# Optimization experiments

Measured on AMD Instinct MI355X. Metric: run time of the kernel, lower is better.

The kernel has to match this reference:

```python
import jax, jax.numpy as jnp
import numpy as np

N_NODES = 50000
N_EDGES = 800000
DIMS = [128, 512, 256, 128]
EPS = 1e-5


def setup_inputs() -> dict:
    key = jax.random.key(0)
    ks = jax.random.split(key, 2 + 5 * 3)
    inp = {
        "x": jax.random.normal(ks[0], (N_NODES, DIMS[0]), dtype=jnp.float32),
        "edge_index": jax.random.randint(ks[1], (2, N_EDGES), 0, N_NODES, dtype=jnp.int64),
    }
    ki = 2
    for i in range(3):
        din, dout = DIMS[i], DIMS[i + 1]
        s = 1.0 / np.sqrt(din)
        inp[f"Wl{i}"] = jax.random.uniform(ks[ki + 0], (din, dout), jnp.float32, -s, s)
        inp[f"bl{i}"] = jax.random.uniform(ks[ki + 1], (dout,), jnp.float32, -s, s)
        inp[f"Wr{i}"] = jax.random.uniform(ks[ki + 2], (din, dout), jnp.float32, -s, s)
        inp[f"g{i}"] = jnp.ones((dout,), jnp.float32)
        inp[f"b{i}"] = jnp.zeros((dout,), jnp.float32)
        ki += 5
    return inp


def _sage_mean(x, src, dst, Wl, bl, Wr):
    n = x.shape[0]
    agg = jax.ops.segment_sum(x[src], dst, num_segments=n)  # [N, din]
    deg = jax.ops.segment_sum(jnp.ones((src.shape[0],), x.dtype), dst, num_segments=n)
    mean = agg / jnp.maximum(deg, 1.0)[:, None]
    return mean @ Wl + bl + x @ Wr


def _bn(h, gamma, beta):
    m = h.mean(axis=0)
    v = h.var(axis=0)
    return gamma * (h - m) * jax.lax.rsqrt(v + EPS) + beta


def reference(x, edge_index, Wl0, bl0, Wr0, g0, b0, Wl1, bl1, Wr1, g1, b1, Wl2, bl2, Wr2, g2, b2):
    src, dst = edge_index[0], edge_index[1]
    params = [(Wl0, bl0, Wr0, g0, b0), (Wl1, bl1, Wr1, g1, b1), (Wl2, bl2, Wr2, g2, b2)]
    h = x
    for Wl, bl, Wr, g, b in params:
        h = _sage_mean(h, src, dst, Wl, bl, Wr)
        h = _bn(h, g, b)
        h = jax.nn.relu(h)
        # dropout: identity in eval mode
    return h
```

## Files before the change

kernel.cpp:

```cpp
#include <hip/hip_runtime.h>
#include <cstdint>
#include <cstddef>


#define EPS_BN 1e-5f

typedef unsigned short ushort_t;
typedef __attribute__((ext_vector_type(8))) short short8;
typedef __attribute__((ext_vector_type(4))) float float4v;
typedef __attribute__((ext_vector_type(2))) float float2v;
typedef __attribute__((ext_vector_type(2))) unsigned int uint2v;
typedef __attribute__((ext_vector_type(4))) unsigned int uint4v;

__device__ __forceinline__ float bflo(unsigned int w) {
    union { unsigned int i; float f; } v; v.i = w << 16; return v.f;
}
__device__ __forceinline__ float bfhi(unsigned int w) {
    union { unsigned int i; float f; } v; v.i = w & 0xffff0000u; return v.f;
}
__device__ __forceinline__ ushort_t f2bf(float f) {
    union { float f; unsigned int i; } v; v.f = f;
    unsigned int r = v.i + 0x7fffu + ((v.i >> 16) & 1u);
    return (ushort_t)(r >> 16);
}

__device__ __forceinline__ void async_copy16(void* lds, const void* g) {
    __builtin_amdgcn_global_load_lds(
        (const __attribute__((address_space(1))) unsigned int*)g,
        (__attribute__((address_space(3))) unsigned int*)lds, 16, 0, 0);
}

__device__ __forceinline__ void edge_sd(const int* __restrict__ p, int e, int ne,
                                        bool is64, int& s, int& d) {
    if (is64) { s = p[2 * e];  d = p[2 * ne + 2 * e]; }
    else      { s = p[e];      d = p[ne + e]; }
}
__device__ __forceinline__ int edge_d(const int* __restrict__ p, int e, int ne, bool is64) {
    return is64 ? p[2 * ne + 2 * e] : p[ne + e];
}

__device__ __forceinline__ bool detect_is64(const int* __restrict__ edges,
                                            int* sh_flag, int t) {
    if (t == 0) *sh_flag = 1;
    __syncthreads();
    if (t < 64 && edges[2 * t + 1] != 0) *sh_flag = 0;
    __syncthreads();
    return *sh_flag != 0;
}

#define EPB 2048

__global__ __launch_bounds__(256) void bhist_kernel(
    const int* __restrict__ edges, int ne, int* __restrict__ gcnt) {
    __shared__ int h[256];
    __shared__ int f64;
    int t = threadIdx.x;
    bool is64 = detect_is64(edges, &f64, t);
    h[t] = 0;
    __syncthreads();
    int base_e = blockIdx.x * EPB;
    #pragma unroll
    for (int u = 0; u < EPB / 256; ++u) {
        int i = base_e + u * 256 + t;
        if (i < ne) atomicAdd(&h[edge_d(edges, i, ne, is64) >> 8], 1);
    }
    __syncthreads();
    if (h[t]) atomicAdd(&gcnt[t], h[t]);
}

__global__ __launch_bounds__(256) void bscan_kernel(
    const int* __restrict__ gcnt, int nb, int ne,
    int* __restrict__ bbase, int* __restrict__ bcur) {
    __shared__ int sh[256];
    int t = threadIdx.x;
    int v = (t < nb) ? gcnt[t] : 0;
    sh[t] = v;
    __syncthreads();
    for (int o = 1; o < 256; o <<= 1) {
        int x = (t >= o) ? sh[t - o] : 0;
        __syncthreads();
        sh[t] += x;
        __syncthreads();
    }
    int excl = sh[t] - v;
    if (t < nb) { bbase[t] = excl; bcur[t] = excl; }
    if (t == nb) bbase[t] = ne;
    if (t == 0 && nb == 256) bbase[256] = ne;
}

__global__ __launch_bounds__(256) void bscatter_kernel(
    const int* __restrict__ edges, int ne,
    int* __restrict__ bcur, int* __restrict__ packed) {
    __shared__ int h[256];
    __shared__ int chunkb[256];
    __shared__ int lcur[256];
    __shared__ int f64;
    int t = threadIdx.x;
    bool is64 = detect_is64(edges, &f64, t);
    h[t] = 0;
    lcur[t] = 0;
    __syncthreads();
    int base_e = blockIdx.x * EPB;
    int ent[EPB / 256], eb[EPB / 256];
    #pragma unroll
    for (int u = 0; u < EPB / 256; ++u) {
        int i = base_e + u * 256 + t;
        if (i < ne) {
            int s, d;
            edge_sd(edges, i, ne, is64, s, d);
            ent[u] = s | ((d & 255) << 24);
            eb[u] = d >> 8;
            atomicAdd(&h[eb[u]], 1);
        } else eb[u] = -1;
    }
    __syncthreads();
    if (h[t]) chunkb[t] = atomicAdd(&bcur[t], h[t]);
    __syncthreads();
    #pragma unroll
    for (int u = 0; u < EPB / 256; ++u) {
        if (eb[u] >= 0) {
            int lp = atomicAdd(&lcur[eb[u]], 1);
            packed[chunkb[eb[u]] + lp] = ent[u];
        }
    }
}

__global__ __launch_bounds__(256) void bbuild_kernel(
    const int* __restrict__ packed, const int* __restrict__ bbase,
    int* __restrict__ rowptr, int* __restrict__ csr_src, int n) {
    __shared__ int h[256];
    __shared__ int cur[256];
    int t = threadIdx.x;
    int bb = blockIdx.x;
    int base = bbase[bb], cnt = bbase[bb + 1] - base;
    h[t] = 0;
    __syncthreads();
    for (int i = t; i < cnt; i += 256)
        atomicAdd(&h[(unsigned)packed[base + i] >> 24], 1);
    __syncthreads();
    int v = h[t];
    for (int o = 1; o < 256; o <<= 1) {
        int x = (t >= o) ? h[t - o] : 0;
        __syncthreads();
        h[t] += x;
        __syncthreads();
    }
    int excl = h[t] - v;
    int node = bb * 256 + t;
    if (node <= n) rowptr[node] = base + excl;
    cur[t] = excl;
    __syncthreads();
    for (int i = t; i < cnt; i += 256) {
        int e = packed[base + i];
        int lp = atomicAdd(&cur[(unsigned)e >> 24], 1);
        csr_src[base + lp] = e & 0xffffff;
    }
}

__global__ void prep_all_kernel(
    const float* __restrict__ x, ushort_t* __restrict__ xb, int nxb,
    const float* __restrict__ Wl0, const float* __restrict__ Wr0,
    ushort_t* __restrict__ WT0, int nb0,
    const float* __restrict__ Wl1, const float* __restrict__ Wr1,
    ushort_t* __restrict__ WT1c, int nb1,
    const float* __restrict__ Wl2, const float* __restrict__ Wr2,
    ushort_t* __restrict__ WT2c) {
    const int D0 = 128, D1 = 512, D2 = 256, D3 = 128;
    int b = blockIdx.x;
    if (b < nxb) {
        int i = b * 256 + threadIdx.x;
        xb[i] = f2bf(x[i]);
        return;
    }
    b -= nxb;
    if (b < nb0) {
        int idx = b * 256 + threadIdx.x;
        int K2 = 2 * D0;
        int nn = idx / K2, k = idx - nn * K2;
        float v = (k < D0) ? Wl0[(size_t)k * D1 + nn] : Wr0[(size_t)(k - D0) * D1 + nn];
        WT0[idx] = f2bf(v);
        return;
    }
    b -= nb0;
    if (b < nb1) {
        int idx = b * 256 + threadIdx.x;
        int nn = idx / D1, k = idx - nn * D1;
        float v = (nn < D2) ? Wl1[(size_t)k * D2 + nn] : Wr1[(size_t)k * D2 + (nn - D2)];
        WT1c[idx] = f2bf(v);
        return;
    }
    b -= nb1;
    {
        int idx = b * 256 + threadIdx.x;
        int nn = idx / D2, k = idx - nn * D2;
        float v = (nn < D3) ? Wl2[(size_t)k * D3 + nn] : Wr2[(size_t)k * D3 + (nn - D3)];
        WT2c[idx] = f2bf(v);
    }
}

template <int VEC> struct VecT;
template <> struct VecT<2> { using T = unsigned int; };
template <> struct VecT<4> { using T = uint2v; };
template <> struct VecT<8> { using T = uint4v; };

template <int VEC>
__device__ __forceinline__ void vunpack(typename VecT<VEC>::T v, unsigned int* w) {
    if constexpr (VEC == 2) { w[0] = v; }
    else if constexpr (VEC == 4) { w[0] = v.x; w[1] = v.y; }
    else { w[0] = v.x; w[1] = v.y; w[2] = v.z; w[3] = v.w; }
}

template <int VEC>
__device__ __forceinline__ void vaccum(typename VecT<VEC>::T v, float* acc) {
    unsigned int w[VEC / 2];
    vunpack<VEC>(v, w);
    #pragma unroll
    for (int i = 0; i < VEC / 2; ++i) {
        acc[2 * i + 0] += bflo(w[i]);
        acc[2 * i + 1] += bfhi(w[i]);
    }
}

template <int VEC>
__device__ __forceinline__ void gather_sum(
    const ushort_t* __restrict__ base, const int* __restrict__ csr_src,
    int e0, int e1, int rstride, float* acc) {
    using VT = typename VecT<VEC>::T;
    int e = e0;
    for (; e + 16 <= e1; e += 16) {
        VT v[16];
        #pragma unroll
        for (int u = 0; u < 16; ++u)
            v[u] = *(const VT*)(base + (size_t)csr_src[e + u] * rstride);
        #pragma unroll
        for (int u = 0; u < 16; ++u) vaccum<VEC>(v[u], acc);
    }
    if (e + 8 <= e1) {
        VT v[8];
        #pragma unroll
        for (int u = 0; u < 8; ++u)
            v[u] = *(const VT*)(base + (size_t)csr_src[e + u] * rstride);
        #pragma unroll
        for (int u = 0; u < 8; ++u) vaccum<VEC>(v[u], acc);
        e += 8;
    }
    if (e + 4 <= e1) {
        VT v[4];
        #pragma unroll
        for (int u = 0; u < 4; ++u)
            v[u] = *(const VT*)(base + (size_t)csr_src[e + u] * rstride);
        #pragma unroll
        for (int u = 0; u < 4; ++u) vaccum<VEC>(v[u], acc);
        e += 4;
    }
    if (e + 2 <= e1) {
        VT v0 = *(const VT*)(base + (size_t)csr_src[e] * rstride);
        VT v1 = *(const VT*)(base + (size_t)csr_src[e + 1] * rstride);
        vaccum<VEC>(v0, acc); vaccum<VEC>(v1, acc);
        e += 2;
    }
    if (e < e1)
        vaccum<VEC>(*(const VT*)(base + (size_t)csr_src[e] * rstride), acc);
}

template <int VEC>
__global__ __launch_bounds__(256) void aggregate_wave_kernel(
    const ushort_t* __restrict__ h, ushort_t* __restrict__ mean,
    const int* __restrict__ rowptr, const int* __restrict__ csr_src, int nnodes) {
    const int din = VEC * 64;
    const int wave = threadIdx.x >> 6;
    const int lane = threadIdx.x & 63;
    const int wstride = gridDim.x * 4;
    using VT = typename VecT<VEC>::T;
    for (int wid = blockIdx.x * 4 + wave; wid < nnodes; wid += wstride) {
        int e0 = rowptr[wid], e1 = rowptr[wid + 1];
        float acc[VEC];
        #pragma unroll
        for (int i = 0; i < VEC; ++i) acc[i] = 0.f;
        gather_sum<VEC>(h + (size_t)lane * VEC, csr_src, e0, e1, din, acc);

        int deg = e1 - e0;
        float scale = 1.0f / (float)(deg > 1 ? deg : 1);
        unsigned int o[VEC / 2];
        #pragma unroll
        for (int i = 0; i < VEC / 2; ++i)
            o[i] = (unsigned int)f2bf(acc[2 * i] * scale) |
                   ((unsigned int)f2bf(acc[2 * i + 1] * scale) << 16);
        VT ov;
        if constexpr (VEC == 2) { ov = o[0]; }
        else if constexpr (VEC == 4) { ov.x = o[0]; ov.y = o[1]; }
        else { ov.x = o[0]; ov.y = o[1]; ov.z = o[2]; ov.w = o[3]; }
        *(VT*)(mean + (size_t)wid * din + (size_t)lane * VEC) = ov;
    }
}

template <int VEC>
__global__ __launch_bounds__(256) void aggregate_add_kernel(
    const ushort_t* __restrict__ PR, const float* __restrict__ bias,
    ushort_t* __restrict__ pre,
    const int* __restrict__ rowptr, const int* __restrict__ csr_src, int nnodes,
    float* __restrict__ gsum, float* __restrict__ gsq) {
    const int D = VEC * 64;
    const int stride = 2 * D;
    __shared__ float s_red[2][4][VEC * 64];
    const int wave = threadIdx.x >> 6;
    const int lane = threadIdx.x & 63;
    const int wstride = gridDim.x * 4;
    using VT = typename VecT<VEC>::T;

    float ssum[VEC], ssq[VEC];
    #pragma unroll
    for (int i = 0; i < VEC; ++i) { ssum[i] = 0.f; ssq[i] = 0.f; }

    for (int wid = blockIdx.x * 4 + wave; wid < nnodes; wid += wstride) {
        int e0 = rowptr[wid], e1 = rowptr[wid + 1];
        float acc[VEC];
        #pragma unroll
        for (int i = 0; i < VEC; ++i) acc[i] = 0.f;
        gather_sum<VEC>(PR + (size_t)lane * VEC, csr_src, e0, e1, stride, acc);

        int deg = e1 - e0;
        float scale = 1.0f / (float)(deg > 1 ? deg : 1);

        VT rv = __builtin_nontemporal_load((const VT*)(PR + (size_t)wid * stride + D + (size_t)lane * VEC));
        unsigned int rw[VEC / 2];
        vunpack<VEC>(rv, rw);
        float o[VEC];
        #pragma unroll
        for (int i = 0; i < VEC / 2; ++i) {
            o[2 * i + 0] = bflo(rw[i]);
            o[2 * i + 1] = bfhi(rw[i]);
        }
        #pragma unroll
        for (int i = 0; i < VEC; ++i) {
            o[i] += acc[i] * scale + bias[lane * VEC + i];
            ssum[i] += o[i];
            ssq[i] += o[i] * o[i];
        }

        unsigned int ow[VEC / 2];
        #pragma unroll
        for (int i = 0; i < VEC / 2; ++i)
            ow[i] = (unsigned int)f2bf(o[2 * i]) | ((unsigned int)f2bf(o[2 * i + 1]) << 16);
        VT ov;
        if constexpr (VEC == 2) { ov = ow[0]; }
        else if constexpr (VEC == 4) { ov.x = ow[0]; ov.y = ow[1]; }
        else { ov.x = ow[0]; ov.y = ow[1]; ov.z = ow[2]; ov.w = ow[3]; }
        __builtin_nontemporal_store(ov, (VT*)(pre + (size_t)wid * D + (size_t)lane * VEC));
    }

    #pragma unroll
    for (int i = 0; i < VEC; ++i) {
        s_red[0][wave][lane * VEC + i] = ssum[i];
        s_red[1][wave][lane * VEC + i] = ssq[i];
    }
    __syncthreads();
    int t = threadIdx.x;
    if (t < D) {
        float a = s_red[0][0][t] + s_red[0][1][t] + s_red[0][2][t] + s_red[0][3][t];
        float q = s_red[1][0][t] + s_red[1][1][t] + s_red[1][2][t] + s_red[1][3][t];
        atomicAdd(&gsum[t], a);
        atomicAdd(&gsq[t], q);
    }
}

template <bool DUAL, bool BIAS, bool STATS>
__global__ __launch_bounds__(512) void gemm_glds_kernel(
    const ushort_t* __restrict__ A1, const ushort_t* __restrict__ A2,
    const ushort_t* __restrict__ BT, const float* __restrict__ bias,
    ushort_t* __restrict__ Cb, int N, int K1, int Ktot, int Wtot,
    float* __restrict__ gsum, float* __restrict__ gsq) {
    __shared__ ushort_t As[256 * 64];
    __shared__ ushort_t Bs[128 * 64];

    const int tid = threadIdx.x;
    const int wave = tid >> 6;
    const int lane = tid & 63;
    const int quad = lane >> 4;
    const int l15 = lane & 15;
    const int sw7 = l15 & 7;
    const int rowBase = blockIdx.y * 256;
    const int colBase = blockIdx.x * 128;
    const int wm = (wave >> 1) * 64;
    const int wn = (wave & 1) * 64;

    float4v acc[4][4];
    #pragma unroll
    for (int i = 0; i < 4; ++i)
        #pragma unroll
        for (int j = 0; j < 4; ++j)
            acc[i][j] = (float4v){0.f, 0.f, 0.f, 0.f};

    const int nkt = Ktot / 64;
    const int khalf = K1 / 64;

    for (int kt = 0; kt < nkt; ++kt) {
        const ushort_t* Asrc = A1;
        int kg = kt * 64;
        if (DUAL && kt >= khalf) { Asrc = A2; kg = (kt - khalf) * 64; }
        const int kb = kt * 64;

        #pragma unroll
        for (int u = 0; u < 4; ++u) {
            int c = u * 512 + tid;
            int r = c >> 3, cc = c & 7;
            int off = (cc ^ (r & 7)) * 8;
            int grow = rowBase + r;
            if (grow >= N) grow = N - 1;
            async_copy16(&As[c * 8], Asrc + (size_t)grow * K1 + kg + off);
        }
        #pragma unroll
        for (int u = 0; u < 2; ++u) {
            int c = u * 512 + tid;
            int r = c >> 3, cc = c & 7;
            int off = (cc ^ (r & 7)) * 8;
            async_copy16(&Bs[c * 8], BT + (size_t)(colBase + r) * Ktot + kb + off);
        }
        __syncthreads();

        #pragma unroll
        for (int kh = 0; kh < 2; ++kh) {
            int cidx = kh * 4 + quad;
            short8 af[4], bf4[4];
            #pragma unroll
            for (int i = 0; i < 4; ++i)
                af[i] = *(const short8*)&As[(wm + i * 16 + l15) * 64 + (cidx ^ sw7) * 8];
            #pragma unroll
            for (int j = 0; j < 4; ++j)
                bf4[j] = *(const short8*)&Bs[(wn + j * 16 + l15) * 64 + (cidx ^ sw7) * 8];
            #pragma unroll
            for (int i = 0; i < 4; ++i)
                #pragma unroll
                for (int j = 0; j < 4; ++j)
                    acc[i][j] = __builtin_amdgcn_mfma_f32_16x16x32_bf16(bf4[j], af[i], acc[i][j], 0, 0, 0);
        }
        __syncthreads();
    }

    float cs[4][4], cq[4][4];
    if constexpr (STATS) {
        #pragma unroll
        for (int j = 0; j < 4; ++j)
            #pragma unroll
            for (int r = 0; r < 4; ++r) { cs[j][r] = 0.f; cq[j][r] = 0.f; }
    }

    ushort_t* lws = &As[wave * 2048];
    #pragma unroll
    for (int p = 0; p < 2; ++p) {
        #pragma unroll
        for (int jj = 0; jj < 2; ++jj) {
            int j = 2 * p + jj;
            float4 bv = make_float4(0.f, 0.f, 0.f, 0.f);
            if (BIAS) bv = *(const float4*)(bias + colBase + wn + j * 16 + quad * 4);
            #pragma unroll
            for (int i = 0; i < 4; ++i) {
                float v0 = acc[i][j][0] + bv.x;
                float v1 = acc[i][j][1] + bv.y;
                float v2 = acc[i][j][2] + bv.z;
                float v3 = acc[i][j][3] + bv.w;
                if constexpr (STATS) {
                    if (rowBase + wm + i * 16 + l15 < N) {
                        cs[j][0] += v0; cq[j][0] += v0 * v0;
                        cs[j][1] += v1; cq[j][1] += v1 * v1;
                        cs[j][2] += v2; cq[j][2] += v2 * v2;
                        cs[j][3] += v3; cq[j][3] += v3 * v3;
                    }
                }
                uint2 pk;
                pk.x = (unsigned int)f2bf(v0) | ((unsigned int)f2bf(v1) << 16);
                pk.y = (unsigned int)f2bf(v2) | ((unsigned int)f2bf(v3) << 16);
                *(uint2*)&lws[(i * 16 + l15) * 32 + jj * 16 + quad * 4] = pk;
            }
        }
        __syncthreads();
        #pragma unroll
        for (int it = 0; it < 4; ++it) {
            int c = it * 64 + lane;
            int row = c >> 2, coff = (c & 3) * 8;
            int grow = rowBase + wm + row;
            if (grow < N) {
                uint4 v = *(const uint4*)&lws[row * 32 + coff];
                *(uint4*)(Cb + (size_t)grow * Wtot + colBase + wn + p * 32 + coff) = v;
            }
        }
        __syncthreads();
    }

    if constexpr (STATS) {
        #pragma unroll
        for (int j = 0; j < 4; ++j)
            #pragma unroll
            for (int r = 0; r < 4; ++r) {
                #pragma unroll
                for (int m = 1; m < 16; m <<= 1) {
                    cs[j][r] += __shfl_xor(cs[j][r], m);
                    cq[j][r] += __shfl_xor(cq[j][r], m);
                }
            }
        if (l15 == 0) {
            #pragma unroll
            for (int j = 0; j < 4; ++j)
                #pragma unroll
                for (int r = 0; r < 4; ++r) {
                    int col = colBase + wn + j * 16 + quad * 4 + r;
                    atomicAdd(&gsum[col], cs[j][r]);
                    atomicAdd(&gsq[col], cq[j][r]);
                }
        }
    }
}

__global__ void bn_relu_b2b_kernel(const ushort_t* __restrict__ h, ushort_t* __restrict__ hb,
                                   int N, int D,
                                   const float* __restrict__ sum, const float* __restrict__ sumsq,
                                   const float* __restrict__ g, const float* __restrict__ b) {
    size_t idx = (size_t)blockIdx.x * blockDim.x + threadIdx.x;
    size_t tot = (size_t)N * D / 2;
    if (idx >= tot) return;
    int cp = (int)(idx & (size_t)(D / 2 - 1));
    int c0 = cp * 2, c1 = c0 + 1;
    float m0 = sum[c0] / (float)N, m1 = sum[c1] / (float)N;
    float i0 = rsqrtf(sumsq[c0] / (float)N - m0 * m0 + EPS_BN);
    float i1 = rsqrtf(sumsq[c1] / (float)N - m1 * m1 + EPS_BN);
    unsigned int w = __builtin_nontemporal_load(&((const unsigned int*)h)[idx]);
    float v0 = g[c0] * (bflo(w) - m0) * i0 + b[c0];
    float v1 = g[c1] * (bfhi(w) - m1) * i1 + b[c1];
    v0 = v0 > 0.f ? v0 : 0.f;
    v1 = v1 > 0.f ? v1 : 0.f;
    ((unsigned int*)hb)[idx] = (unsigned int)f2bf(v0) | ((unsigned int)f2bf(v1) << 16);
}

__global__ void bn_relu_b2f_kernel(const ushort_t* __restrict__ h, float* __restrict__ hf,
                                   int N, int D,
                                   const float* __restrict__ sum, const float* __restrict__ sumsq,
                                   const float* __restrict__ g, const float* __restrict__ b) {
    size_t idx = (size_t)blockIdx.x * blockDim.x + threadIdx.x;
    size_t tot = (size_t)N * D / 2;
    if (idx >= tot) return;
    int cp = (int)(idx & (size_t)(D / 2 - 1));
    int c0 = cp * 2, c1 = c0 + 1;
    float m0 = sum[c0] / (float)N, m1 = sum[c1] / (float)N;
    float i0 = rsqrtf(sumsq[c0] / (float)N - m0 * m0 + EPS_BN);
    float i1 = rsqrtf(sumsq[c1] / (float)N - m1 * m1 + EPS_BN);
    unsigned int w = __builtin_nontemporal_load(&((const unsigned int*)h)[idx]);
    float v0 = g[c0] * (bflo(w) - m0) * i0 + b[c0];
    float v1 = g[c1] * (bfhi(w) - m1) * i1 + b[c1];
    float2v o;
    o.x = v0 > 0.f ? v0 : 0.f;
    o.y = v1 > 0.f ? v1 : 0.f;
    __builtin_nontemporal_store(o, (float2v*)(hf + idx * 2));
}

extern "C" void kernel_launch(void* const* d_in, const int* in_sizes, int n_in,
                              void* d_out, int out_size, void* d_ws, size_t ws_size,
                              hipStream_t stream) {
    const float* x     = (const float*)d_in[0];
    const int*   edges = (const int*)d_in[1];
    const float* Wl0 = (const float*)d_in[2];
    const float* bl0 = (const float*)d_in[3];
    const float* Wr0 = (const float*)d_in[4];
    const float* g0  = (const float*)d_in[5];
    const float* b0  = (const float*)d_in[6];
    const float* Wl1 = (const float*)d_in[7];
    const float* bl1 = (const float*)d_in[8];
    const float* Wr1 = (const float*)d_in[9];
    const float* g1  = (const float*)d_in[10];
    const float* b1  = (const float*)d_in[11];
    const float* Wl2 = (const float*)d_in[12];
    const float* bl2 = (const float*)d_in[13];
    const float* Wr2 = (const float*)d_in[14];
    const float* g2  = (const float*)d_in[15];
    const float* b2  = (const float*)d_in[16];

    const int D0 = 128, D1 = 512, D2 = 256, D3 = 128;
    const int n  = in_sizes[0] / D0;
    const int ne = in_sizes[1] / 2;
    const int NB = (n + 255) >> 8;

    char* base = (char*)d_ws;
    size_t off = 0;
    auto alloc = [&](size_t bytes) -> char* {
        char* p = base + off;
        off = (off + bytes + 255) & ~(size_t)255;
        return p;
    };
    int*      gcnt    = (int*)alloc(256 * 4);
    float*    stats   = (float*)alloc(6 * 512 * 4);
    size_t    zero_span = off;
    int*      bbase   = (int*)alloc(257 * 4);
    int*      bcur    = (int*)alloc(256 * 4);
    int*      packed  = (int*)alloc((size_t)ne * 4);
    int*      rowptr  = (int*)alloc((size_t)(n + 1) * 4);
    int*      csr_src = (int*)alloc((size_t)ne * 4);
    ushort_t* xb      = (ushort_t*)alloc((size_t)n * D0 * 2);
    ushort_t* mb      = (ushort_t*)alloc((size_t)n * 512 * 2);
    ushort_t* h1b     = (ushort_t*)alloc((size_t)n * D1 * 2);
    ushort_t* h2b     = (ushort_t*)alloc((size_t)n * D2 * 2);
    ushort_t* hpre    = (ushort_t*)alloc((size_t)n * 512 * 2);
    ushort_t* WT0     = (ushort_t*)alloc((size_t)D1 * 2 * D0 * 2);
    ushort_t* WT1c    = (ushort_t*)alloc((size_t)(2 * D2) * D1 * 2);
    ushort_t* WT2c    = (ushort_t*)alloc((size_t)(2 * D3) * D2 * 2);
    float*    out     = (float*)d_out;
    (void)ws_size; (void)n_in; (void)out_size;

    hipMemsetAsync(base, 0, zero_span, stream);

    int ablk = (ne + EPB - 1) / EPB;
    bhist_kernel<<<ablk, 256, 0, stream>>>(edges, ne, gcnt);
    bscan_kernel<<<1, 256, 0, stream>>>(gcnt, NB, ne, bbase, bcur);
    bscatter_kernel<<<ablk, 256, 0, stream>>>(edges, ne, bcur, packed);
    bbuild_kernel<<<NB, 256, 0, stream>>>(packed, bbase, rowptr, csr_src, n);

    const int nxb = (n * D0) / 256;
    const int nb0 = (D1 * 2 * D0) / 256;
    const int nb1 = (2 * D2 * D1) / 256;
    const int nb2 = (2 * D3 * D2) / 256;
    prep_all_kernel<<<nxb + nb0 + nb1 + nb2, 256, 0, stream>>>(
        x, xb, nxb, Wl0, Wr0, WT0, nb0, Wl1, Wr1, WT1c, nb1, Wl2, Wr2, WT2c);

    const int aggGrid = 2048;
    const int rowBlocks = (n + 255) / 256;
    float* st0 = stats + 0 * 1024;
    float* st1 = stats + 1 * 1024;
    float* st2 = stats + 2 * 1024;

    aggregate_wave_kernel<2><<<aggGrid, 256, 0, stream>>>(xb, mb, rowptr, csr_src, n);
    gemm_glds_kernel<true, true, true><<<dim3(D1 / 128, rowBlocks), 512, 0, stream>>>(
        mb, xb, WT0, bl0, hpre, n, D0, 2 * D0, D1, st0, st0 + 512);
    bn_relu_b2b_kernel<<<((size_t)n * D1 / 2 + 255) / 256, 256, 0, stream>>>(
        hpre, h1b, n, D1, st0, st0 + 512, g0, b0);

    gemm_glds_kernel<false, false, false><<<dim3(2 * D2 / 128, rowBlocks), 512, 0, stream>>>(
        h1b, nullptr, WT1c, nullptr, mb, n, D1, D1, 2 * D2, nullptr, nullptr);
    aggregate_add_kernel<4><<<aggGrid, 256, 0, stream>>>(
        mb, bl1, hpre, rowptr, csr_src, n, st1, st1 + 512);
    bn_relu_b2b_kernel<<<((size_t)n * D2 / 2 + 255) / 256, 256, 0, stream>>>(
        hpre, h2b, n, D2, st1, st1 + 512, g1, b1);

    gemm_glds_kernel<false, false, false><<<dim3(2 * D3 / 128, rowBlocks), 512, 0, stream>>>(
        h2b, nullptr, WT2c, nullptr, mb, n, D2, D2, 2 * D3, nullptr, nullptr);
    aggregate_add_kernel<2><<<aggGrid, 256, 0, stream>>>(
        mb, bl2, hpre, rowptr, csr_src, n, st2, st2 + 512);
    bn_relu_b2f_kernel<<<((size_t)n * D3 / 2 + 255) / 256, 256, 0, stream>>>(
        hpre, out, n, D3, st2, st2 + 512, g2, b2);
}
```

Measured before the change: 587.1 us.

## Double-buffer GEMM LDS tiles with K=32 stages and drop nontemporal hints

The bf16 MFMA GEMM now splits K into 32-wide stages held in two LDS buffers. The next stage's async copies are issued before computing the current one, using explicit vmcnt waits and barriers, and MFMA issue priority is raised during the compute block. The aim is to hide global-to-LDS latency behind compute instead of stalling on a full sync every iteration, at the cost of more barriers and shorter MFMA bursts. Separately, the nontemporal load/store hints in the aggregation and BN kernels are replaced with plain accesses so intermediates can stay in cache.

```diff
diff --git a/kernel.cpp b/kernel.cpp
--- a/kernel.cpp
+++ b/kernel.cpp
@@ -322,7 +322,7 @@
         int deg = e1 - e0;
         float scale = 1.0f / (float)(deg > 1 ? deg : 1);
 
-        VT rv = __builtin_nontemporal_load((const VT*)(PR + (size_t)wid * stride + D + (size_t)lane * VEC));
+        VT rv = *(const VT*)(PR + (size_t)wid * stride + D + (size_t)lane * VEC);
         unsigned int rw[VEC / 2];
         vunpack<VEC>(rv, rw);
         float o[VEC];
@@ -346,7 +346,7 @@
         if constexpr (VEC == 2) { ov = ow[0]; }
         else if constexpr (VEC == 4) { ov.x = ow[0]; ov.y = ow[1]; }
         else { ov.x = ow[0]; ov.y = ow[1]; ov.z = ow[2]; ov.w = ow[3]; }
-        __builtin_nontemporal_store(ov, (VT*)(pre + (size_t)wid * D + (size_t)lane * VEC));
+        *(VT*)(pre + (size_t)wid * D + (size_t)lane * VEC) = ov;
     }
 
     #pragma unroll
@@ -370,15 +370,15 @@
     const ushort_t* __restrict__ BT, const float* __restrict__ bias,
     ushort_t* __restrict__ Cb, int N, int K1, int Ktot, int Wtot,
     float* __restrict__ gsum, float* __restrict__ gsq) {
-    __shared__ ushort_t As[256 * 64];
-    __shared__ ushort_t Bs[128 * 64];
+    __shared__ ushort_t As[2 * 256 * 32];
+    __shared__ ushort_t Bs[2 * 128 * 32];
 
     const int tid = threadIdx.x;
     const int wave = tid >> 6;
     const int lane = tid & 63;
     const int quad = lane >> 4;
     const int l15 = lane & 15;
-    const int sw7 = l15 & 7;
+    const int sw3 = l15 & 3;
     const int rowBase = blockIdx.y * 256;
     const int colBase = blockIdx.x * 128;
     const int wm = (wave >> 1) * 64;
@@ -391,50 +391,57 @@
         for (int j = 0; j < 4; ++j)
             acc[i][j] = (float4v){0.f, 0.f, 0.f, 0.f};
 
-    const int nkt = Ktot / 64;
-    const int khalf = K1 / 64;
-
-    for (int kt = 0; kt < nkt; ++kt) {
+    const int nkt = Ktot / 32;
+    const int khalf = K1 / 32;
+
+    auto stage = [&](int buf, int kt) {
         const ushort_t* Asrc = A1;
-        int kg = kt * 64;
-        if (DUAL && kt >= khalf) { Asrc = A2; kg = (kt - khalf) * 64; }
-        const int kb = kt * 64;
-
-        #pragma unroll
-        for (int u = 0; u < 4; ++u) {
+        int kg = kt * 32;
+        if (DUAL && kt >= khalf) { Asrc = A2; kg = (kt - khalf) * 32; }
+        const int kb = kt * 32;
+        #pragma unroll
+        for (int u = 0; u < 2; ++u) {
             int c = u * 512 + tid;
-            int r = c >> 3, cc = c & 7;
-            int off = (cc ^ (r & 7)) * 8;
+            int r = c >> 2, cc = c & 3;
+            int off = (cc ^ (r & 3)) * 8;
             int grow = rowBase + r;
             if (grow >= N) grow = N - 1;
-            async_copy16(&As[c * 8], Asrc + (size_t)grow * K1 + kg + off);
-        }
-        #pragma unroll
-        for (int u = 0; u < 2; ++u) {
-            int c = u * 512 + tid;
-            int r = c >> 3, cc = c & 7;
-            int off = (cc ^ (r & 7)) * 8;
-            async_copy16(&Bs[c * 8], BT + (size_t)(colBase + r) * Ktot + kb + off);
-        }
-        __syncthreads();
-
-        #pragma unroll
-        for (int kh = 0; kh < 2; ++kh) {
-            int cidx = kh * 4 + quad;
-            short8 af[4], bf4[4];
-            #pragma unroll
-            for (int i = 0; i < 4; ++i)
-                af[i] = *(const short8*)&As[(wm + i * 16 + l15) * 64 + (cidx ^ sw7) * 8];
+            async_copy16(&As[buf * 8192 + c * 8], Asrc + (size_t)grow * K1 + kg + off);
+        }
+        {
+            int c = tid;
+            int r = c >> 2, cc = c & 3;
+            int off = (cc ^ (r & 3)) * 8;
+            async_copy16(&Bs[buf * 4096 + c * 8], BT + (size_t)(colBase + r) * Ktot + kb + off);
+        }
+    };
+
+    stage(0, 0);
+    int cur = 0;
+    for (int kt = 0; kt < nkt; ++kt) {
+        if (kt + 1 < nkt) {
+            stage(cur ^ 1, kt + 1);
+            asm volatile("s_waitcnt vmcnt(3)\n\ts_barrier" ::: "memory");
+        } else {
+            asm volatile("s_waitcnt vmcnt(0)\n\ts_barrier" ::: "memory");
+        }
+
+        short8 af[4], bf4[4];
+        #pragma unroll
+        for (int i = 0; i < 4; ++i)
+            af[i] = *(const short8*)&As[cur * 8192 + (wm + i * 16 + l15) * 32 + (quad ^ sw3) * 8];
+        #pragma unroll
+        for (int j = 0; j < 4; ++j)
+            bf4[j] = *(const short8*)&Bs[cur * 4096 + (wn + j * 16 + l15) * 32 + (quad ^ sw3) * 8];
+        __builtin_amdgcn_s_setprio(1);
+        #pragma unroll
+        for (int i = 0; i < 4; ++i)
             #pragma unroll
             for (int j = 0; j < 4; ++j)
-                bf4[j] = *(const short8*)&Bs[(wn + j * 16 + l15) * 64 + (cidx ^ sw7) * 8];
-            #pragma unroll
-            for (int i = 0; i < 4; ++i)
-                #pragma unroll
-                for (int j = 0; j < 4; ++j)
-                    acc[i][j] = __builtin_amdgcn_mfma_f32_16x16x32_bf16(bf4[j], af[i], acc[i][j], 0, 0, 0);
-        }
-        __syncthreads();
+                acc[i][j] = __builtin_amdgcn_mfma_f32_16x16x32_bf16(bf4[j], af[i], acc[i][j], 0, 0, 0);
+        __builtin_amdgcn_s_setprio(0);
+        asm volatile("s_barrier" ::: "memory");
+        cur ^= 1;
     }
 
     float cs[4][4], cq[4][4];
@@ -523,7 +530,7 @@
     float m0 = sum[c0] / (float)N, m1 = sum[c1] / (float)N;
     float i0 = rsqrtf(sumsq[c0] / (float)N - m0 * m0 + EPS_BN);
     float i1 = rsqrtf(sumsq[c1] / (float)N - m1 * m1 + EPS_BN);
-    unsigned int w = __builtin_nontemporal_load(&((const unsigned int*)h)[idx]);
+    unsigned int w = ((const unsigned int*)h)[idx];
     float v0 = g[c0] * (bflo(w) - m0) * i0 + b[c0];
     float v1 = g[c1] * (bfhi(w) - m1) * i1 + b[c1];
     v0 = v0 > 0.f ? v0 : 0.f;
@@ -543,13 +550,13 @@
     float m0 = sum[c0] / (float)N, m1 = sum[c1] / (float)N;
     float i0 = rsqrtf(sumsq[c0] / (float)N - m0 * m0 + EPS_BN);
     float i1 = rsqrtf(sumsq[c1] / (float)N - m1 * m1 + EPS_BN);
-    unsigned int w = __builtin_nontemporal_load(&((const unsigned int*)h)[idx]);
+    unsigned int w = ((const unsigned int*)h)[idx];
     float v0 = g[c0] * (bflo(w) - m0) * i0 + b[c0];
     float v1 = g[c1] * (bfhi(w) - m1) * i1 + b[c1];
     float2v o;
     o.x = v0 > 0.f ? v0 : 0.f;
     o.y = v1 > 0.f ? v1 : 0.f;
-    __builtin_nontemporal_store(o, (float2v*)(hf + idx * 2));
+    *(float2v*)(hf + idx * 2) = o;
 }
 
 extern "C" void kernel_launch(void* const* d_in, const int* in_sizes, int n_in,
```

Result: slower. 607.0 us (+3.4%).

## Double-buffer GEMM LDS tiles with 128x128 blocks and drop nontemporal hints

Applied to the files above, without the earlier changes.

The GEMM moves from a 256x128 tile with 512 threads and one shared buffer to 128x128 tiles with 256 threads, two LDS buffers and two blocks per CU. The next k-tile is prefetched while the current one runs its MFMAs, with explicit vmcnt waits, and MFMA priority is raised, to hide global-load latency behind compute. Nontemporal loads and stores in the aggregate and BN kernels become plain accesses so intermediates can stay in cache. The inline-asm barrier and vmcnt counting are fragile and depend on how the compiler orders the copies.

```diff
diff --git a/kernel.cpp b/kernel.cpp
--- a/kernel.cpp
+++ b/kernel.cpp
@@ -322,7 +322,7 @@
         int deg = e1 - e0;
         float scale = 1.0f / (float)(deg > 1 ? deg : 1);
 
-        VT rv = __builtin_nontemporal_load((const VT*)(PR + (size_t)wid * stride + D + (size_t)lane * VEC));
+        VT rv = *(const VT*)(PR + (size_t)wid * stride + D + (size_t)lane * VEC);
         unsigned int rw[VEC / 2];
         vunpack<VEC>(rv, rw);
         float o[VEC];
@@ -346,7 +346,7 @@
         if constexpr (VEC == 2) { ov = ow[0]; }
         else if constexpr (VEC == 4) { ov.x = ow[0]; ov.y = ow[1]; }
         else { ov.x = ow[0]; ov.y = ow[1]; ov.z = ow[2]; ov.w = ow[3]; }
-        __builtin_nontemporal_store(ov, (VT*)(pre + (size_t)wid * D + (size_t)lane * VEC));
+        *(VT*)(pre + (size_t)wid * D + (size_t)lane * VEC) = ov;
     }
 
     #pragma unroll
@@ -365,13 +365,13 @@
 }
 
 template <bool DUAL, bool BIAS, bool STATS>
-__global__ __launch_bounds__(512) void gemm_glds_kernel(
+__global__ __launch_bounds__(256, 2) void gemm_glds_kernel(
     const ushort_t* __restrict__ A1, const ushort_t* __restrict__ A2,
     const ushort_t* __restrict__ BT, const float* __restrict__ bias,
     ushort_t* __restrict__ Cb, int N, int K1, int Ktot, int Wtot,
     float* __restrict__ gsum, float* __restrict__ gsq) {
-    __shared__ ushort_t As[256 * 64];
-    __shared__ ushort_t Bs[128 * 64];
+    __shared__ ushort_t As[2 * 128 * 64];
+    __shared__ ushort_t Bs[2 * 128 * 64];
 
     const int tid = threadIdx.x;
     const int wave = tid >> 6;
@@ -379,7 +379,7 @@
     const int quad = lane >> 4;
     const int l15 = lane & 15;
     const int sw7 = l15 & 7;
-    const int rowBase = blockIdx.y * 256;
+    const int rowBase = blockIdx.y * 128;
     const int colBase = blockIdx.x * 128;
     const int wm = (wave >> 1) * 64;
     const int wn = (wave & 1) * 64;
@@ -394,29 +394,38 @@
     const int nkt = Ktot / 64;
     const int khalf = K1 / 64;
 
-    for (int kt = 0; kt < nkt; ++kt) {
+    auto stage = [&](int buf, int kt) {
         const ushort_t* Asrc = A1;
         int kg = kt * 64;
         if (DUAL && kt >= khalf) { Asrc = A2; kg = (kt - khalf) * 64; }
         const int kb = kt * 64;
-
         #pragma unroll
         for (int u = 0; u < 4; ++u) {
-            int c = u * 512 + tid;
+            int c = u * 256 + tid;
             int r = c >> 3, cc = c & 7;
             int off = (cc ^ (r & 7)) * 8;
             int grow = rowBase + r;
             if (grow >= N) grow = N - 1;
-            async_copy16(&As[c * 8], Asrc + (size_t)grow * K1 + kg + off);
-        }
-        #pragma unroll
-        for (int u = 0; u < 2; ++u) {
-            int c = u * 512 + tid;
+            async_copy16(&As[buf * 8192 + c * 8], Asrc + (size_t)grow * K1 + kg + off);
+        }
+        #pragma unroll
+        for (int u = 0; u < 4; ++u) {
+            int c = u * 256 + tid;
             int r = c >> 3, cc = c & 7;
             int off = (cc ^ (r & 7)) * 8;
-            async_copy16(&Bs[c * 8], BT + (size_t)(colBase + r) * Ktot + kb + off);
-        }
-        __syncthreads();
+            async_copy16(&Bs[buf * 8192 + c * 8], BT + (size_t)(colBase + r) * Ktot + kb + off);
+        }
+    };
+
+    stage(0, 0);
+    int cur = 0;
+    for (int kt = 0; kt < nkt; ++kt) {
+        if (kt + 1 < nkt) {
+            stage(cur ^ 1, kt + 1);
+            asm volatile("s_waitcnt vmcnt(8)\n\ts_barrier" ::: "memory");
+        } else {
+            asm volatile("s_waitcnt vmcnt(0)\n\ts_barrier" ::: "memory");
+        }
 
         #pragma unroll
         for (int kh = 0; kh < 2; ++kh) {
@@ -424,17 +433,20 @@
             short8 af[4], bf4[4];
             #pragma unroll
             for (int i = 0; i < 4; ++i)
-                af[i] = *(const short8*)&As[(wm + i * 16 + l15) * 64 + (cidx ^ sw7) * 8];
+                af[i] = *(const short8*)&As[cur * 8192 + (wm + i * 16 + l15) * 64 + (cidx ^ sw7) * 8];
             #pragma unroll
             for (int j = 0; j < 4; ++j)
-                bf4[j] = *(const short8*)&Bs[(wn + j * 16 + l15) * 64 + (cidx ^ sw7) * 8];
+                bf4[j] = *(const short8*)&Bs[cur * 8192 + (wn + j * 16 + l15) * 64 + (cidx ^ sw7) * 8];
+            __builtin_amdgcn_s_setprio(1);
             #pragma unroll
             for (int i = 0; i < 4; ++i)
                 #pragma unroll
                 for (int j = 0; j < 4; ++j)
                     acc[i][j] = __builtin_amdgcn_mfma_f32_16x16x32_bf16(bf4[j], af[i], acc[i][j], 0, 0, 0);
-        }
-        __syncthreads();
+            __builtin_amdgcn_s_setprio(0);
+        }
+        asm volatile("s_barrier" ::: "memory");
+        cur ^= 1;
     }
 
     float cs[4][4], cq[4][4];
@@ -523,7 +535,7 @@
     float m0 = sum[c0] / (float)N, m1 = sum[c1] / (float)N;
     float i0 = rsqrtf(sumsq[c0] / (float)N - m0 * m0 + EPS_BN);
     float i1 = rsqrtf(sumsq[c1] / (float)N - m1 * m1 + EPS_BN);
-    unsigned int w = __builtin_nontemporal_load(&((const unsigned int*)h)[idx]);
+    unsigned int w = ((const unsigned int*)h)[idx];
     float v0 = g[c0] * (bflo(w) - m0) * i0 + b[c0];
     float v1 = g[c1] * (bfhi(w) - m1) * i1 + b[c1];
     v0 = v0 > 0.f ? v0 : 0.f;
@@ -543,13 +555,13 @@
     float m0 = sum[c0] / (float)N, m1 = sum[c1] / (float)N;
     float i0 = rsqrtf(sumsq[c0] / (float)N - m0 * m0 + EPS_BN);
     float i1 = rsqrtf(sumsq[c1] / (float)N - m1 * m1 + EPS_BN);
-    unsigned int w = __builtin_nontemporal_load(&((const unsigned int*)h)[idx]);
+    unsigned int w = ((const unsigned int*)h)[idx];
     float v0 = g[c0] * (bflo(w) - m0) * i0 + b[c0];
     float v1 = g[c1] * (bfhi(w) - m1) * i1 + b[c1];
     float2v o;
     o.x = v0 > 0.f ? v0 : 0.f;
     o.y = v1 > 0.f ? v1 : 0.f;
-    __builtin_nontemporal_store(o, (float2v*)(hf + idx * 2));
+    *(float2v*)(hf + idx * 2) = o;
 }
 
 extern "C" void kernel_launch(void* const* d_in, const int* in_sizes, int n_in,
@@ -565,8 +577,8 @@
     const float* Wl1 = (const float*)d_in[7];
     const float* bl1 = (const float*)d_in[8];
     const float* Wr1 = (const float*)d_in[9];
+    const float* b1_  = (const float*)d_in[11];
     const float* g1  = (const float*)d_in[10];
-    const float* b1  = (const float*)d_in[11];
     const float* Wl2 = (const float*)d_in[12];
     const float* bl2 = (const float*)d_in[13];
     const float* Wr2 = (const float*)d_in[14];
@@ -620,25 +632,25 @@
         x, xb, nxb, Wl0, Wr0, WT0, nb0, Wl1, Wr1, WT1c, nb1, Wl2, Wr2, WT2c);
 
     const int aggGrid = 2048;
-    const int rowBlocks = (n + 255) / 256;
+    const int rowBlocks = (n + 127) / 128;
     float* st0 = stats + 0 * 1024;
     float* st1 = stats + 1 * 1024;
     float* st2 = stats + 2 * 1024;
 
     aggregate_wave_kernel<2><<<aggGrid, 256, 0, stream>>>(xb, mb, rowptr, csr_src, n);
-    gemm_glds_kernel<true, true, true><<<dim3(D1 / 128, rowBlocks), 512, 0, stream>>>(
+    gemm_glds_kernel<true, true, true><<<dim3(D1 / 128, rowBlocks), 256, 0, stream>>>(
         mb, xb, WT0, bl0, hpre, n, D0, 2 * D0, D1, st0, st0 + 512);
     bn_relu_b2b_kernel<<<((size_t)n * D1 / 2 + 255) / 256, 256, 0, stream>>>(
         hpre, h1b, n, D1, st0, st0 + 512, g0, b0);
 
-    gemm_glds_kernel<false, false, false><<<dim3(2 * D2 / 128, rowBlocks), 512, 0, stream>>>(
+    gemm_glds_kernel<false, false, false><<<dim3(2 * D2 / 128, rowBlocks), 256, 0, stream>>>(
         h1b, nullptr, WT1c, nullptr, mb, n, D1, D1, 2 * D2, nullptr, nullptr);
     aggregate_add_kernel<4><<<aggGrid, 256, 0, stream>>>(
         mb, bl1, hpre, rowptr, csr_src, n, st1, st1 + 512);
     bn_relu_b2b_kernel<<<((size_t)n * D2 / 2 + 255) / 256, 256, 0, stream>>>(
-        hpre, h2b, n, D2, st1, st1 + 512, g1, b1);
-
-    gemm_glds_kernel<false, false, false><<<dim3(2 * D3 / 128, rowBlocks), 512, 0, stream>>>(
+        hpre, h2b, n, D2, st1, st1 + 512, g1, b1_);
+
+    gemm_glds_kernel<false, false, false><<<dim3(2 * D3 / 128, rowBlocks), 256, 0, stream>>>(
         h2b, nullptr, WT2c, nullptr, mb, n, D2, D2, 2 * D3, nullptr, nullptr);
     aggregate_add_kernel<2><<<aggGrid, 256, 0, stream>>>(
         mb, bl2, hpre, rowptr, csr_src, n, st2, st2 + 512);
```

Result: no change. 595.9 us (+1.5%).
